# Kernel optimization log

Hardware: AMD Instinct MI355X
Metric: run time of the kernel (lower is better)

The kernel has to match this reference:

```python
import jax, jax.numpy as jnp
import numpy as np

B, T, I, H, V = 32, 64, 512, 512, 32000


def setup_inputs() -> dict:
    key = jax.random.key(0)
    ks = jax.random.split(key, 8)
    s_in = 1.0 / np.sqrt(H)  # torch LSTMCell/Linear uniform init scale
    return {
        "isequence": jax.random.normal(ks[0], (B, T, I), dtype=jnp.float32),
        "hidden_t": jax.random.normal(ks[1], (B, H), dtype=jnp.float32),
        "W_ih": jax.random.uniform(ks[2], (4 * H, I), jnp.float32, -s_in, s_in),
        "W_hh": jax.random.uniform(ks[3], (4 * H, H), jnp.float32, -s_in, s_in),
        "b_ih": jax.random.uniform(ks[4], (4 * H,), jnp.float32, -s_in, s_in),
        "b_hh": jax.random.uniform(ks[5], (4 * H,), jnp.float32, -s_in, s_in),
        "W_out": jax.random.uniform(ks[6], (V, H), jnp.float32, -s_in, s_in),
        "b_out": jax.random.uniform(ks[7], (V,), jnp.float32, -s_in, s_in),
    }


def reference(isequence, hidden_t, W_ih, W_hh, b_ih, b_hh, W_out, b_out):
    # isequence: [B, T, I] -> time-major [T, B, I] (matches permute(1,0,2))
    xs = jnp.transpose(isequence, (1, 0, 2))
    # Precompute input-to-gate projections for all timesteps: [T, B, 4H]
    x_gates = jnp.einsum("tbi,gi->tbg", xs, W_ih) + b_ih + b_hh
    c0 = jnp.zeros_like(hidden_t)  # init_hidden zeros cell state

    def step(carry, xg):
        h, c = carry
        gates = xg + h @ W_hh.T  # [B, 4H], torch gate order: i, f, g, o
        i_g, f_g, g_g, o_g = jnp.split(gates, 4, axis=-1)
        i_g = jax.nn.sigmoid(i_g)
        f_g = jax.nn.sigmoid(f_g)
        g_g = jnp.tanh(g_g)
        o_g = jax.nn.sigmoid(o_g)
        c_new = f_g * c + i_g * g_g
        h_new = o_g * jnp.tanh(c_new)
        logits = h_new @ W_out.T + b_out  # [B, V]
        return (h_new, c_new), logits

    _, osequence = jax.lax.scan(step, (hidden_t, c0), x_gates)  # [T, B, V]
    return jnp.transpose(osequence, (1, 0, 2))  # [B, T, V]
```

## Files before the change

### kernel.cpp

```cpp
#include <hip/hip_runtime.h>
#include <hip/hip_bf16.h>

typedef unsigned short u16;
typedef unsigned int u32;
typedef __attribute__((ext_vector_type(4))) float f32x4;
typedef __attribute__((ext_vector_type(8))) short short8;
typedef __attribute__((ext_vector_type(4))) unsigned short u16x4;
typedef __attribute__((ext_vector_type(4))) unsigned int u32x4;

#define LSTM_NBLK 16
#define LSTM_GRID 240

static __device__ __forceinline__ u16 f2bf(float f) {
  union { float f; unsigned u; } v; v.f = f;
  unsigned r = v.u + 0x7FFFu + ((v.u >> 16) & 1u);
  return (u16)(r >> 16);
}

static __device__ __forceinline__ void gload_lds16(const void* g, void* l) {
  __builtin_amdgcn_global_load_lds(
      (const __attribute__((address_space(1))) unsigned int*)g,
      (__attribute__((address_space(3))) unsigned int*)l, 16, 0, 0);
}

static __device__ __forceinline__ short8 ld_b128_sc(const void* p) {
  short8 r;
  asm volatile("global_load_dwordx4 %0, %1, off sc0 sc1"
               : "=v"(r) : "v"(p) : "memory");
  return r;
}
static __device__ __forceinline__ unsigned ld_u32_sc_wait(const unsigned* p) {
  unsigned r;
  asm volatile("global_load_dword %0, %1, off sc0 sc1\n\ts_waitcnt vmcnt(0)"
               : "=v"(r) : "v"(p) : "memory");
  return r;
}
static __device__ __forceinline__ void st_u32_sc(void* p, unsigned v) {
  asm volatile("global_store_dword %0, %1, off sc0 sc1"
               :: "v"(p), "v"(v) : "memory");
}
static __device__ __forceinline__ void waitcnt0() {
  asm volatile("s_waitcnt vmcnt(0)" ::: "memory");
  __builtin_amdgcn_sched_barrier(0);
}

__global__ void prep_kernel(const float* __restrict__ iseq, const float* __restrict__ h0,
                            const float* __restrict__ wih, const float* __restrict__ whh,
                            u16* __restrict__ wih_bf, u16* __restrict__ whh_bf,
                            u16* __restrict__ ax, u32* __restrict__ h2u,
                            unsigned* __restrict__ flags) {
  const int S0 = 262144;
  const int S1 = S0 + 262144;
  const int S2 = S1 + 262144;
  const int S3 = S2 + 8192;
  const int S4 = S3 + 4096;
  int u = blockIdx.x * blockDim.x + threadIdx.x;
  int stride = gridDim.x * blockDim.x;
  for (; u < S4; u += stride) {
    if (u < S0) {
      int e = u * 4; f32x4 v = *(const f32x4*)(wih + e);
      u16x4 o; o[0]=f2bf(v[0]); o[1]=f2bf(v[1]); o[2]=f2bf(v[2]); o[3]=f2bf(v[3]);
      *(u16x4*)(wih_bf + e) = o;
    } else if (u < S1) {
      int e = (u - S0) * 4; f32x4 v = *(const f32x4*)(whh + e);
      u16x4 o; o[0]=f2bf(v[0]); o[1]=f2bf(v[1]); o[2]=f2bf(v[2]); o[3]=f2bf(v[3]);
      *(u16x4*)(whh_bf + e) = o;
    } else if (u < S2) {
      int e = (u - S1) * 4; int m = e >> 9; int k = e & 511;
      int b = m & 31; int t = m >> 5;
      f32x4 v = *(const f32x4*)(iseq + ((b * 64 + t) << 9) + k);
      u16x4 o; o[0]=f2bf(v[0]); o[1]=f2bf(v[1]); o[2]=f2bf(v[2]); o[3]=f2bf(v[3]);
      *(u16x4*)(ax + e) = o;
    } else if (u < S3) {
      int v = u - S2;
      int e = v * 2;
      float lo = h0[e], hi = h0[e + 1];
      h2u[v] = (((u32)f2bf(hi)) << 16) | (u32)f2bf(lo);
    } else {
      flags[u - S3] = 0u;
    }
  }
}

__global__ __launch_bounds__(256, 2) void gemm_bt(
    const u16* __restrict__ A, const u16* __restrict__ Bw,
    float* __restrict__ C, const float* __restrict__ bias1,
    const float* __restrict__ bias2, int N) {
  __shared__ u16 As[2][8192];
  __shared__ u16 Bs[2][8192];
  const int tid = threadIdx.x;
  const int w = tid >> 6, l = tid & 63;
  const int wr = w >> 1, wc = w & 1;
  const int lid = blockIdx.x;
  const int cpx = gridDim.x >> 3;
  const int lid2 = (lid & 7) * cpx + (lid >> 3);
  const int tn = (lid2 >> 4) * 128;
  const int tm = (lid2 & 15) * 128;

  f32x4 acc[4][4];
#pragma unroll
  for (int i = 0; i < 4; ++i)
#pragma unroll
    for (int j = 0; j < 4; ++j) acc[i][j] = (f32x4){0.f, 0.f, 0.f, 0.f};

  auto stage = [&](int buf, int kt) {
#pragma unroll
    for (int i = 0; i < 4; ++i) {
      int r = (w * 4 + i) * 8 + (l >> 3);
      int c16 = (l & 7) ^ (r & 7);
      const u16* srca = A + (tm + r) * 512 + kt * 64 + c16 * 8;
      gload_lds16(srca, &As[buf][(w * 4 + i) * 512]);
      const u16* srcb = Bw + (tn + r) * 512 + kt * 64 + c16 * 8;
      gload_lds16(srcb, &Bs[buf][(w * 4 + i) * 512]);
    }
  };

  stage(0, 0);
  int buf = 0;
  for (int kt = 0; kt < 8; ++kt) {
    __syncthreads();
    if (kt < 7) stage(buf ^ 1, kt + 1);
#pragma unroll
    for (int kk = 0; kk < 2; ++kk) {
      short8 af[4], bfr[4];
#pragma unroll
      for (int mi = 0; mi < 4; ++mi) {
        int row = wr * 64 + mi * 16 + (l & 15);
        int s = (kk * 4 + (l >> 4)) ^ (row & 7);
        af[mi] = *(const short8*)&As[buf][row * 64 + s * 8];
      }
#pragma unroll
      for (int ni = 0; ni < 4; ++ni) {
        int row = wc * 64 + ni * 16 + (l & 15);
        int s = (kk * 4 + (l >> 4)) ^ (row & 7);
        bfr[ni] = *(const short8*)&Bs[buf][row * 64 + s * 8];
      }
#pragma unroll
      for (int mi = 0; mi < 4; ++mi)
#pragma unroll
        for (int ni = 0; ni < 4; ++ni)
          acc[mi][ni] = __builtin_amdgcn_mfma_f32_16x16x32_bf16(
              af[mi], bfr[ni], acc[mi][ni], 0, 0, 0);
    }
    buf ^= 1;
  }

#pragma unroll
  for (int ni = 0; ni < 4; ++ni) {
    int gcol = tn + wc * 64 + ni * 16 + (l & 15);
    float bv = 0.f;
    if (bias1) bv += bias1[gcol];
    if (bias2) bv += bias2[gcol];
#pragma unroll
    for (int mi = 0; mi < 4; ++mi) {
      int grow0 = tm + wr * 64 + mi * 16 + ((l >> 4) << 2);
      f32x4 a = acc[mi][ni];
#pragma unroll
      for (int q = 0; q < 4; ++q) {
        C[(long long)(grow0 + q) * N + gcol] = a[q] + bv;
      }
    }
  }
}

__global__ __launch_bounds__(512, 1) void gemm2_256(
    const u16* __restrict__ A, const u16* __restrict__ Bw,
    float* __restrict__ C, const float* __restrict__ bias, int N) {
  __shared__ u16 Asl[3][16384];
  __shared__ u16 Bsl[3][8192];
  const int tid = threadIdx.x;
  const int w = tid >> 6, l = tid & 63;
  const int wr = w >> 1, wc = w & 1;
  const int lid = blockIdx.x;
  const int cpx = gridDim.x >> 3;
  const int lid2 = (lid & 7) * cpx + (lid >> 3);
  const int tm = (lid2 & 7) * 256;
  const int tn = (lid2 >> 3) * 128;

  f32x4 acc[4][4];
#pragma unroll
  for (int i = 0; i < 4; ++i)
#pragma unroll
    for (int j = 0; j < 4; ++j) acc[i][j] = (f32x4){0.f, 0.f, 0.f, 0.f};

  auto stage = [&](int slot, int kt) {
#pragma unroll
    for (int j = 0; j < 4; ++j) {
      int chunk = w * 4 + j;
      int r = chunk * 8 + (l >> 3);
      int c16 = (l & 7) ^ (r & 7);
      int rowm = tm + r;
      const u16* srca = A + ((rowm & 63) + 1) * 16384 + (rowm >> 6) * 512
                          + kt * 64 + c16 * 8;
      gload_lds16(srca, &Asl[slot][chunk * 512]);
    }
#pragma unroll
    for (int j = 0; j < 2; ++j) {
      int chunk = w * 2 + j;
      int r = chunk * 8 + (l >> 3);
      int c16 = (l & 7) ^ (r & 7);
      const u16* srcb = Bw + (tn + r) * 512 + kt * 64 + c16 * 8;
      gload_lds16(srcb, &Bsl[slot][chunk * 512]);
    }
  };

  stage(0, 0);
  stage(1, 1);
  for (int kt = 0; kt < 8; ++kt) {
    const int slot = kt % 3;
    if (kt < 7) {
      asm volatile("s_waitcnt vmcnt(6)" ::: "memory");
    } else {
      asm volatile("s_waitcnt vmcnt(0)" ::: "memory");
    }
    __builtin_amdgcn_sched_barrier(0);
    __builtin_amdgcn_s_barrier();
    __builtin_amdgcn_sched_barrier(0);
    if (kt < 6) stage((kt + 2) % 3, kt + 2);
#pragma unroll
    for (int kk = 0; kk < 2; ++kk) {
      short8 bfr[4];
#pragma unroll
      for (int ni = 0; ni < 4; ++ni) {
        int row = wc * 64 + ni * 16 + (l & 15);
        int s = (kk * 4 + (l >> 4)) ^ (row & 7);
        bfr[ni] = *(const short8*)&Bsl[slot][row * 64 + s * 8];
      }
#pragma unroll
      for (int mi = 0; mi < 4; ++mi) {
        int row = wr * 64 + mi * 16 + (l & 15);
        int s = (kk * 4 + (l >> 4)) ^ (row & 7);
        short8 af = *(const short8*)&Asl[slot][row * 64 + s * 8];
#pragma unroll
        for (int ni = 0; ni < 4; ++ni)
          acc[mi][ni] = __builtin_amdgcn_mfma_f32_16x16x32_bf16(
              af, bfr[ni], acc[mi][ni], 0, 0, 0);
      }
    }
  }

#pragma unroll
  for (int ni = 0; ni < 4; ++ni) {
    int gcol = tn + wc * 64 + ni * 16 + (l & 15);
    float bv = bias[gcol];
#pragma unroll
    for (int mi = 0; mi < 4; ++mi) {
      int grow0 = tm + wr * 64 + mi * 16 + ((l >> 4) << 2);
      f32x4 a = acc[mi][ni];
#pragma unroll
      for (int q = 0; q < 4; ++q) {
        C[(long long)(grow0 + q) * N + gcol] = a[q] + bv;
      }
    }
  }
}

__global__ __launch_bounds__(512, 1) void lstm_persist(
    const u16* __restrict__ whh, const float* __restrict__ xg,
    u16* __restrict__ h2, unsigned* __restrict__ flags,
    const float* __restrict__ wout, u16* __restrict__ wout_bf) {
  __shared__ u16 hbuf[32 * 512];
  __shared__ u16 hloc[1024];
  const int tid = threadIdx.x;

  if (blockIdx.x >= LSTM_NBLK) {
    int idx = (blockIdx.x - LSTM_NBLK) * 512 + tid;
    int stride = (LSTM_GRID - LSTM_NBLK) * 512;
    for (int u2 = idx; u2 < 4096000; u2 += stride) {
      int e = u2 * 4; f32x4 v = *(const f32x4*)(wout + e);
      u16x4 o; o[0]=f2bf(v[0]); o[1]=f2bf(v[1]); o[2]=f2bf(v[2]); o[3]=f2bf(v[3]);
      *(u16x4*)(wout_bf + e) = o;
    }
    return;
  }

  const int w = tid >> 6, l = tid & 63;
  const int blk = blockIdx.x;
  const int j0 = (blk * 8 + w) * 4;
  const int c = l & 15;
  const int wrow = (c >> 2) * 512 + j0 + (c & 3);
  const int ko = (l >> 4) * 8;
  u32* h2u = (u32*)h2;

  short8 bfr[16];
  const u16* wp = whh + wrow * 512 + ko;
#pragma unroll
  for (int kt = 0; kt < 16; ++kt) bfr[kt] = *(const short8*)(wp + kt * 32);

  const int rq = (l >> 4) * 4;
  const int jj = l & 3;
  const int b0 = l & 15, b1 = 16 + (l & 15);
  const int s0 = b0 & 7;

  const int cb = tid & 31;
  const int ckg = tid >> 5;
  const int csw = cb & 7;

  const int ob = tid >> 4;
  const int oj = tid & 15;

  float creg[2][4];
#pragma unroll
  for (int mt = 0; mt < 2; ++mt)
#pragma unroll
    for (int q = 0; q < 4; ++q) creg[mt][q] = 0.f;

  float xcur[2][4], xnext[2][4];
#pragma unroll
  for (int mt = 0; mt < 2; ++mt)
#pragma unroll
    for (int q = 0; q < 4; ++q)
      xcur[mt][q] = xg[(mt * 16 + rq + q) * 2048 + wrow];

  for (int it = 0; it < 64; ++it) {
    if (it > 0) {
      const unsigned want = (unsigned)it;
      const unsigned* fl = flags + blk * 256 + ckg * 16;
      for (;;) {
        unsigned f = ld_u32_sc_wait(fl);
        if (__all((int)(f >= want))) break;
      }
    }
    {
      const u16* src = h2 + it * 16384 + cb * 512 + ckg * 32;
      short8 d0 = ld_b128_sc(src);
      short8 d1 = ld_b128_sc(src + 8);
      short8 d2 = ld_b128_sc(src + 16);
      short8 d3 = ld_b128_sc(src + 24);
      waitcnt0();
      *(short8*)&hbuf[cb * 512 + (((ckg * 4 + 0) ^ csw) * 8)] = d0;
      *(short8*)&hbuf[cb * 512 + (((ckg * 4 + 1) ^ csw) * 8)] = d1;
      *(short8*)&hbuf[cb * 512 + (((ckg * 4 + 2) ^ csw) * 8)] = d2;
      *(short8*)&hbuf[cb * 512 + (((ckg * 4 + 3) ^ csw) * 8)] = d3;
    }
    __syncthreads();

    f32x4 acc0 = (f32x4){0.f, 0.f, 0.f, 0.f};
    f32x4 acc1 = (f32x4){0.f, 0.f, 0.f, 0.f};
#pragma unroll
    for (int kt = 0; kt < 16; ++kt) {
      int x = ((kt * 4 + (l >> 4)) ^ s0) * 8;
      short8 a0 = *(const short8*)&hbuf[b0 * 512 + x];
      short8 a1 = *(const short8*)&hbuf[b1 * 512 + x];
      acc0 = __builtin_amdgcn_mfma_f32_16x16x32_bf16(a0, bfr[kt], acc0, 0, 0, 0);
      acc1 = __builtin_amdgcn_mfma_f32_16x16x32_bf16(a1, bfr[kt], acc1, 0, 0, 0);
    }
    if (it < 63) {
#pragma unroll
      for (int mt = 0; mt < 2; ++mt)
#pragma unroll
        for (int q = 0; q < 4; ++q)
          xnext[mt][q] = xg[((it + 1) * 32 + mt * 16 + rq + q) * 2048 + wrow];
    }

#pragma unroll
    for (int mt = 0; mt < 2; ++mt) {
#pragma unroll
      for (int q = 0; q < 4; ++q) {
        float av = (mt == 0) ? acc0[q] : acc1[q];
        float gp = av + xcur[mt][q];
        int bl = (l & 48) | jj;
        float xi = __shfl(gp, bl);
        float xf = __shfl(gp, bl | 4);
        float xgg = __shfl(gp, bl | 8);
        float xo = __shfl(gp, bl | 12);
        float is = 1.f / (1.f + __expf(-xi));
        float fs = 1.f / (1.f + __expf(-xf));
        float e2 = __expf(2.f * xgg);
        float gt = 1.f - 2.f / (e2 + 1.f);
        float os = 1.f / (1.f + __expf(-xo));
        float cn = fs * creg[mt][q] + is * gt;
        creg[mt][q] = cn;
        float e2c = __expf(2.f * cn);
        float hn = os * (1.f - 2.f / (e2c + 1.f));
        if ((l & 12) == 0) {
          int b = mt * 16 + rq + q;
          hloc[b * 32 + w * 4 + jj] = f2bf(hn);
        }
      }
    }
    __syncthreads();

    {
      u32 v = *(const u32*)&hloc[ob * 32 + oj * 2];
      st_u32_sc(h2u + (it + 1) * 8192 + ob * 256 + blk * 16 + oj, v);
      waitcnt0();
    }
    __syncthreads();

    if (it < 63) {
      if (w == 0 && l < 16)
        st_u32_sc(flags + l * 256 + blk * 16, (unsigned)(it + 1));
#pragma unroll
      for (int mt = 0; mt < 2; ++mt)
#pragma unroll
        for (int q = 0; q < 4; ++q)
          xcur[mt][q] = xnext[mt][q];
    }
  }
}

extern "C" void kernel_launch(void* const* d_in, const int* in_sizes, int n_in,
                              void* d_out, int out_size, void* d_ws, size_t ws_size,
                              hipStream_t stream) {
  (void)in_sizes; (void)n_in; (void)out_size; (void)ws_size;
  const float* iseq = (const float*)d_in[0];
  const float* h0   = (const float*)d_in[1];
  const float* wih  = (const float*)d_in[2];
  const float* whh  = (const float*)d_in[3];
  const float* bih  = (const float*)d_in[4];
  const float* bhh  = (const float*)d_in[5];
  const float* wout = (const float*)d_in[6];
  const float* bout = (const float*)d_in[7];

  char* ws = (char*)d_ws;
  u16* wout_bf = (u16*)(ws + 0);
  u16* wih_bf  = (u16*)(ws + 32768000);
  u16* whh_bf  = (u16*)(ws + 34865152);
  u16* ax      = (u16*)(ws + 36962304);
  u16* h2      = (u16*)(ws + 39059456);
  unsigned* flags = (unsigned*)(ws + 41189376);
  float* xg    = (float*)(ws + 41254912);
  float* out   = (float*)d_out;

  prep_kernel<<<2048, 256, 0, stream>>>(iseq, h0, wih, whh,
                                        wih_bf, whh_bf, ax, (u32*)h2, flags);
  gemm_bt<<<256, 256, 0, stream>>>(ax, wih_bf, xg, bih, bhh, 2048);
  lstm_persist<<<LSTM_GRID, 512, 0, stream>>>(whh_bf, xg, h2, flags,
                                              wout, wout_bf);
  gemm2_256<<<2000, 512, 0, stream>>>(h2, wout_bf, out, bout, 32000);
}
```

Before: 524.5 us.

## Replace LSTM step flags with step-tagged hidden-state words in persistent kernel

Each bf16 hidden value is now stored in a 32-bit word whose upper half carries the timestep tag. Consumers spin on the tagged data itself instead of polling a separate flag array, which removes the store-wait, extra barrier and flag store from each step. A block reads its own slice of h from LDS instead of global memory. The cost is twice the bytes for the hidden-state exchange and a second store of plain packed h for the output GEMM.

Result: slower. 643.0 us (+22.6%).

```diff
diff --git a/kernel.cpp b/kernel.cpp
--- a/kernel.cpp
+++ b/kernel.cpp
@@ -6,6 +6,7 @@
 typedef __attribute__((ext_vector_type(4))) float f32x4;
 typedef __attribute__((ext_vector_type(8))) short short8;
 typedef __attribute__((ext_vector_type(4))) unsigned short u16x4;
+typedef __attribute__((ext_vector_type(2))) unsigned int u32x2;
 typedef __attribute__((ext_vector_type(4))) unsigned int u32x4;
 
 #define LSTM_NBLK 16
@@ -23,13 +24,13 @@
       (__attribute__((address_space(3))) unsigned int*)l, 16, 0, 0);
 }
 
-static __device__ __forceinline__ short8 ld_b128_sc(const void* p) {
-  short8 r;
+static __device__ __forceinline__ u32x4 ld_b128u_sc(const u32* p) {
+  u32x4 r;
   asm volatile("global_load_dwordx4 %0, %1, off sc0 sc1"
                : "=v"(r) : "v"(p) : "memory");
   return r;
 }
-static __device__ __forceinline__ unsigned ld_u32_sc_wait(const unsigned* p) {
+static __device__ __forceinline__ unsigned ld_u32_sc_wait(const u32* p) {
   unsigned r;
   asm volatile("global_load_dword %0, %1, off sc0 sc1\n\ts_waitcnt vmcnt(0)"
                : "=v"(r) : "v"(p) : "memory");
@@ -39,6 +40,11 @@
   asm volatile("global_store_dword %0, %1, off sc0 sc1"
                :: "v"(p), "v"(v) : "memory");
 }
+static __device__ __forceinline__ void st_u64_sc(void* p, u32 lo, u32 hi) {
+  u32x2 v; v[0] = lo; v[1] = hi;
+  asm volatile("global_store_dwordx2 %0, %1, off sc0 sc1"
+               :: "v"(p), "v"(v) : "memory");
+}
 static __device__ __forceinline__ void waitcnt0() {
   asm volatile("s_waitcnt vmcnt(0)" ::: "memory");
   __builtin_amdgcn_sched_barrier(0);
@@ -47,16 +53,17 @@
 __global__ void prep_kernel(const float* __restrict__ iseq, const float* __restrict__ h0,
                             const float* __restrict__ wih, const float* __restrict__ whh,
                             u16* __restrict__ wih_bf, u16* __restrict__ whh_bf,
-                            u16* __restrict__ ax, u32* __restrict__ h2u,
-                            unsigned* __restrict__ flags) {
+                            u16* __restrict__ ax, u32* __restrict__ htag,
+                            u32* __restrict__ h2u) {
   const int S0 = 262144;
   const int S1 = S0 + 262144;
   const int S2 = S1 + 262144;
-  const int S3 = S2 + 8192;
-  const int S4 = S3 + 4096;
+  const int S3 = S2 + 4096;
+  const int S4 = S3 + 258048;
+  const int S5 = S4 + 2048;
   int u = blockIdx.x * blockDim.x + threadIdx.x;
   int stride = gridDim.x * blockDim.x;
-  for (; u < S4; u += stride) {
+  for (; u < S5; u += stride) {
     if (u < S0) {
       int e = u * 4; f32x4 v = *(const f32x4*)(wih + e);
       u16x4 o; o[0]=f2bf(v[0]); o[1]=f2bf(v[1]); o[2]=f2bf(v[2]); o[3]=f2bf(v[3]);
@@ -72,12 +79,26 @@
       u16x4 o; o[0]=f2bf(v[0]); o[1]=f2bf(v[1]); o[2]=f2bf(v[2]); o[3]=f2bf(v[3]);
       *(u16x4*)(ax + e) = o;
     } else if (u < S3) {
-      int v = u - S2;
+      int e = (u - S2) * 4; f32x4 v = *(const f32x4*)(h0 + e);
+      u32x4 o;
+      o[0] = (1u << 16) | f2bf(v[0]); o[1] = (1u << 16) | f2bf(v[1]);
+      o[2] = (1u << 16) | f2bf(v[2]); o[3] = (1u << 16) | f2bf(v[3]);
+      *(u32x4*)(htag + e) = o;
+    } else if (u < S4) {
+      int e = (u - S3) * 4;
+      u32x4 z = {0u, 0u, 0u, 0u};
+      *(u32x4*)(htag + 16384 + e) = z;
+    } else {
+      int v = (u - S4) * 4;
       int e = v * 2;
-      float lo = h0[e], hi = h0[e + 1];
-      h2u[v] = (((u32)f2bf(hi)) << 16) | (u32)f2bf(lo);
-    } else {
-      flags[u - S3] = 0u;
+      f32x4 x0 = *(const f32x4*)(h0 + e);
+      f32x4 x1 = *(const f32x4*)(h0 + e + 4);
+      u32x4 o;
+      o[0] = (((u32)f2bf(x0[1])) << 16) | (u32)f2bf(x0[0]);
+      o[1] = (((u32)f2bf(x0[3])) << 16) | (u32)f2bf(x0[2]);
+      o[2] = (((u32)f2bf(x1[1])) << 16) | (u32)f2bf(x1[0]);
+      o[3] = (((u32)f2bf(x1[3])) << 16) | (u32)f2bf(x1[2]);
+      *(u32x4*)(h2u + v) = o;
     }
   }
 }
@@ -257,7 +278,7 @@
 
 __global__ __launch_bounds__(512, 1) void lstm_persist(
     const u16* __restrict__ whh, const float* __restrict__ xg,
-    u16* __restrict__ h2, unsigned* __restrict__ flags,
+    u32* __restrict__ htag, u32* __restrict__ h2u,
     const float* __restrict__ wout, u16* __restrict__ wout_bf) {
   __shared__ u16 hbuf[32 * 512];
   __shared__ u16 hloc[1024];
@@ -280,7 +301,6 @@
   const int c = l & 15;
   const int wrow = (c >> 2) * 512 + j0 + (c & 3);
   const int ko = (l >> 4) * 8;
-  u32* h2u = (u32*)h2;
 
   short8 bfr[16];
   const u16* wp = whh + wrow * 512 + ko;
@@ -296,8 +316,8 @@
   const int ckg = tid >> 5;
   const int csw = cb & 7;
 
-  const int ob = tid >> 4;
-  const int oj = tid & 15;
+  const int pb = tid >> 4;
+  const int pj = tid & 15;
 
   float creg[2][4];
 #pragma unroll
@@ -313,26 +333,53 @@
       xcur[mt][q] = xg[(mt * 16 + rq + q) * 2048 + wrow];
 
   for (int it = 0; it < 64; ++it) {
+    const unsigned want = (unsigned)(it + 1);
+    const bool ownp = (ckg == blk);
     if (it > 0) {
-      const unsigned want = (unsigned)it;
-      const unsigned* fl = flags + blk * 256 + ckg * 16;
+      const u32* sen = htag + it * 16384 + ckg * 32;
       for (;;) {
-        unsigned f = ld_u32_sc_wait(fl);
-        if (__all((int)(f >= want))) break;
-      }
-    }
-    {
-      const u16* src = h2 + it * 16384 + cb * 512 + ckg * 32;
-      short8 d0 = ld_b128_sc(src);
-      short8 d1 = ld_b128_sc(src + 8);
-      short8 d2 = ld_b128_sc(src + 16);
-      short8 d3 = ld_b128_sc(src + 24);
-      waitcnt0();
-      *(short8*)&hbuf[cb * 512 + (((ckg * 4 + 0) ^ csw) * 8)] = d0;
-      *(short8*)&hbuf[cb * 512 + (((ckg * 4 + 1) ^ csw) * 8)] = d1;
-      *(short8*)&hbuf[cb * 512 + (((ckg * 4 + 2) ^ csw) * 8)] = d2;
-      *(short8*)&hbuf[cb * 512 + (((ckg * 4 + 3) ^ csw) * 8)] = d3;
-    }
+        unsigned f = ownp ? (want << 16) : ld_u32_sc_wait(sen);
+        if (__all((int)((f >> 16) == want))) break;
+      }
+    }
+    short8 d0, d1, d2, d3;
+    if (ownp && it > 0) {
+      d0 = *(const short8*)&hloc[cb * 32 + 0];
+      d1 = *(const short8*)&hloc[cb * 32 + 8];
+      d2 = *(const short8*)&hloc[cb * 32 + 16];
+      d3 = *(const short8*)&hloc[cb * 32 + 24];
+    } else {
+      const u32* src = htag + it * 16384 + cb * 512 + ckg * 32;
+      u32x4 a0, a1, a2, a3, a4, a5, a6, a7;
+      for (;;) {
+        a0 = ld_b128u_sc(src +  0); a1 = ld_b128u_sc(src +  4);
+        a2 = ld_b128u_sc(src +  8); a3 = ld_b128u_sc(src + 12);
+        a4 = ld_b128u_sc(src + 16); a5 = ld_b128u_sc(src + 20);
+        a6 = ld_b128u_sc(src + 24); a7 = ld_b128u_sc(src + 28);
+        waitcnt0();
+        unsigned d = 0;
+#pragma unroll
+        for (int q2 = 0; q2 < 4; ++q2) {
+          d |= (a0[q2] >> 16) ^ want; d |= (a1[q2] >> 16) ^ want;
+          d |= (a2[q2] >> 16) ^ want; d |= (a3[q2] >> 16) ^ want;
+          d |= (a4[q2] >> 16) ^ want; d |= (a5[q2] >> 16) ^ want;
+          d |= (a6[q2] >> 16) ^ want; d |= (a7[q2] >> 16) ^ want;
+        }
+        if (d == 0) break;
+      }
+      d0[0]=(short)a0[0]; d0[1]=(short)a0[1]; d0[2]=(short)a0[2]; d0[3]=(short)a0[3];
+      d0[4]=(short)a1[0]; d0[5]=(short)a1[1]; d0[6]=(short)a1[2]; d0[7]=(short)a1[3];
+      d1[0]=(short)a2[0]; d1[1]=(short)a2[1]; d1[2]=(short)a2[2]; d1[3]=(short)a2[3];
+      d1[4]=(short)a3[0]; d1[5]=(short)a3[1]; d1[6]=(short)a3[2]; d1[7]=(short)a3[3];
+      d2[0]=(short)a4[0]; d2[1]=(short)a4[1]; d2[2]=(short)a4[2]; d2[3]=(short)a4[3];
+      d2[4]=(short)a5[0]; d2[5]=(short)a5[1]; d2[6]=(short)a5[2]; d2[7]=(short)a5[3];
+      d3[0]=(short)a6[0]; d3[1]=(short)a6[1]; d3[2]=(short)a6[2]; d3[3]=(short)a6[3];
+      d3[4]=(short)a7[0]; d3[5]=(short)a7[1]; d3[6]=(short)a7[2]; d3[7]=(short)a7[3];
+    }
+    *(short8*)&hbuf[cb * 512 + (((ckg * 4 + 0) ^ csw) * 8)] = d0;
+    *(short8*)&hbuf[cb * 512 + (((ckg * 4 + 1) ^ csw) * 8)] = d1;
+    *(short8*)&hbuf[cb * 512 + (((ckg * 4 + 2) ^ csw) * 8)] = d2;
+    *(short8*)&hbuf[cb * 512 + (((ckg * 4 + 3) ^ csw) * 8)] = d3;
     __syncthreads();
 
     f32x4 acc0 = (f32x4){0.f, 0.f, 0.f, 0.f};
@@ -382,15 +429,17 @@
     __syncthreads();
 
     {
-      u32 v = *(const u32*)&hloc[ob * 32 + oj * 2];
-      st_u32_sc(h2u + (it + 1) * 8192 + ob * 256 + blk * 16 + oj, v);
-      waitcnt0();
-    }
-    __syncthreads();
-
+      u32 lo = (u32)hloc[pb * 32 + pj * 2];
+      u32 hi = (u32)hloc[pb * 32 + pj * 2 + 1];
+      if (it < 63) {
+        u32 tag = ((u32)(it + 2)) << 16;
+        st_u64_sc(htag + (it + 1) * 16384 + pb * 512 + blk * 32 + pj * 2,
+                  tag | lo, tag | hi);
+      }
+      st_u32_sc(h2u + (it + 1) * 8192 + pb * 256 + blk * 16 + pj,
+                (hi << 16) | lo);
+    }
     if (it < 63) {
-      if (w == 0 && l < 16)
-        st_u32_sc(flags + l * 256 + blk * 16, (unsigned)(it + 1));
 #pragma unroll
       for (int mt = 0; mt < 2; ++mt)
 #pragma unroll
@@ -419,14 +468,14 @@
   u16* whh_bf  = (u16*)(ws + 34865152);
   u16* ax      = (u16*)(ws + 36962304);
   u16* h2      = (u16*)(ws + 39059456);
-  unsigned* flags = (unsigned*)(ws + 41189376);
-  float* xg    = (float*)(ws + 41254912);
+  u32* htag    = (u32*)(ws + 41189376);
+  float* xg    = (float*)(ws + 45383680);
   float* out   = (float*)d_out;
 
   prep_kernel<<<2048, 256, 0, stream>>>(iseq, h0, wih, whh,
-                                        wih_bf, whh_bf, ax, (u32*)h2, flags);
+                                        wih_bf, whh_bf, ax, htag, (u32*)h2);
   gemm_bt<<<256, 256, 0, stream>>>(ax, wih_bf, xg, bih, bhh, 2048);
-  lstm_persist<<<LSTM_GRID, 512, 0, stream>>>(whh_bf, xg, h2, flags,
+  lstm_persist<<<LSTM_GRID, 512, 0, stream>>>(whh_bf, xg, htag, (u32*)h2,
                                               wout, wout_bf);
   gemm2_256<<<2000, 512, 0, stream>>>(h2, wout_bf, out, bout, 32000);
 }
```
